# Kernel tuning notes

Hardware: AMD Instinct MI355X
Metric: run time of the kernel (lower is better)

Reference implementation:

```python
import jax, jax.numpy as jnp
import numpy as np

B, S, D = 2, 2048, 2048
H = 16
HD = D // H  # 128

def setup_inputs() -> dict:
    key = jax.random.key(0)
    k1, k2, k3 = jax.random.split(key, 3)
    x = jax.random.normal(k1, (B, S, D), dtype=jnp.float32)
    w_qkv = jax.random.normal(k2, (D, 3 * D), dtype=jnp.float32) * (1.0 / np.sqrt(D))
    b_qkv = jnp.zeros((3 * D,), dtype=jnp.float32)
    w_out = jax.random.normal(k3, (D, D), dtype=jnp.float32) * (1.0 / np.sqrt(D))
    b_out = jnp.zeros((D,), dtype=jnp.float32)
    return {"x": x, "w_qkv": w_qkv, "b_qkv": b_qkv, "w_out": w_out, "b_out": b_out}

def reference(x, w_qkv, b_qkv, w_out, b_out):
    batch, seq_len, channels = x.shape
    qkv = x @ w_qkv + b_qkv                      # [B,S,3D]
    q, k, v = jnp.split(qkv, 3, axis=-1)
    # [B,S,D] -> [B,H,S,HD]
    def heads(t):
        return t.reshape(batch, seq_len, H, HD).transpose(0, 2, 1, 3)
    q, k, v = heads(q), heads(k), heads(v)
    scale = 1.0 / np.sqrt(HD).astype(np.float32)
    attn = jnp.einsum('bhqd,bhkd->bhqk', q, k) * scale
    causal = jnp.tril(jnp.ones((seq_len, seq_len), dtype=bool))
    attn = jnp.where(causal, attn, -jnp.inf)
    attn = jax.nn.softmax(attn, axis=-1)
    y = jnp.einsum('bhqk,bhkd->bhqd', attn, v)   # [B,H,S,HD]
    y = y.transpose(0, 2, 1, 3).reshape(batch, seq_len, channels)
    return y @ w_out + b_out
```

## Files before the change

### kernel.cpp

```cpp
#include <hip/hip_runtime.h>
#include <hip/hip_bf16.h>
#include <cstdint>
#include <cstddef>

#define BB 2
#define SS 2048
#define DD 2048
#define HH 16
#define HDIM 128
#define QSCALE 0.12751743f

typedef short bf16x8 __attribute__((ext_vector_type(8)));
typedef float f32x4 __attribute__((ext_vector_type(4)));
typedef float f32x16 __attribute__((ext_vector_type(16)));

__device__ __forceinline__ ushort f2bf(float f) {
    union { float f; uint32_t u; } v; v.f = f;
    uint32_t u = v.u;
    u += 0x7fffu + ((u >> 16) & 1u);
    return (ushort)(u >> 16);
}

__device__ __forceinline__ ushort f2bf_fast(float f) {
    union { float f; uint32_t u; } v; v.f = f;
    return (ushort)((v.u + 0x8000u) >> 16);
}

__device__ __forceinline__ void gl16(const ushort* g, ushort* l) {
    __builtin_amdgcn_global_load_lds(
        (const __attribute__((address_space(1))) unsigned int*)g,
        (__attribute__((address_space(3))) unsigned int*)l,
        16, 0, 0);
}

__global__ __launch_bounds__(256) void cast_x_kernel(
    const float* __restrict__ X, ushort* __restrict__ Xb)
{
    size_t idx = ((size_t)blockIdx.x * 256 + threadIdx.x) * 8;
    float4 a = *(const float4*)(X + idx);
    float4 b = *(const float4*)(X + idx + 4);
    ushort4 o0, o1;
    o0.x = f2bf(a.x); o0.y = f2bf(a.y); o0.z = f2bf(a.z); o0.w = f2bf(a.w);
    o1.x = f2bf(b.x); o1.y = f2bf(b.y); o1.z = f2bf(b.z); o1.w = f2bf(b.w);
    *(ushort4*)(Xb + idx) = o0;
    *(ushort4*)(Xb + idx + 4) = o1;
}

__global__ __launch_bounds__(256) void transpose_cast_kernel(
    const float* __restrict__ W, ushort* __restrict__ Wt, int K, int N)
{
    __shared__ ushort tile[32][36];
    const int n0 = blockIdx.x * 32;
    const int k0 = blockIdx.y * 32;
    const int t = threadIdx.x;
    const int r = t >> 3;
    const int c = (t & 7) * 4;
    float4 a = *(const float4*)(W + (size_t)(k0 + r) * N + n0 + c);
    tile[r][c + 0] = f2bf(a.x); tile[r][c + 1] = f2bf(a.y);
    tile[r][c + 2] = f2bf(a.z); tile[r][c + 3] = f2bf(a.w);
    __syncthreads();
    ushort4 o;
    o.x = tile[c + 0][r]; o.y = tile[c + 1][r];
    o.z = tile[c + 2][r]; o.w = tile[c + 3][r];
    *(ushort4*)(Wt + (size_t)(n0 + r) * K + k0 + c) = o;
}

__global__ __launch_bounds__(256) void transpose_v_kernel(
    const ushort* __restrict__ V, ushort* __restrict__ Vt)
{
    __shared__ ushort tile[32][36];
    const int s0 = blockIdx.x * 32;
    const int h0 = blockIdx.y * 32;
    const int bh = blockIdx.z;
    const ushort* Vp = V + (size_t)bh * SS * HDIM;
    ushort* Vtp = Vt + (size_t)bh * HDIM * SS;
    const int t = threadIdx.x;
    const int r = t >> 3;
    const int c = (t & 7) * 4;
    *(ushort4*)&tile[r][c] = *(const ushort4*)(Vp + (size_t)(s0 + r) * HDIM + h0 + c);
    __syncthreads();
    ushort4 o;
    o.x = tile[c + 0][r]; o.y = tile[c + 1][r];
    o.z = tile[c + 2][r]; o.w = tile[c + 3][r];
    *(ushort4*)(Vtp + (size_t)(h0 + r) * SS + s0 + c) = o;
}

__global__ __launch_bounds__(256) void gemm_qkv_kernel(
    const ushort* __restrict__ A, const ushort* __restrict__ Bt,
    const float* __restrict__ bias,
    ushort* __restrict__ Qo, ushort* __restrict__ Ko, ushort* __restrict__ Vo)
{
    const int n0 = blockIdx.x * 128;
    const int m0 = blockIdx.y * 128;
    __shared__ ushort As[128 * 64];
    __shared__ ushort Bs[128 * 64];
    const int t = threadIdx.x, w = t >> 6, lane = t & 63;
    const int l31 = lane & 31, hh = lane >> 5;
    const int wr = w >> 1, wc = w & 1;
    const int l7 = l31 & 7;

    const int rt   = lane >> 3;
    const int koff = ((lane & 7) ^ rt) * 8;

    f32x16 acc[2][2];
#pragma unroll
    for (int i = 0; i < 2; ++i)
#pragma unroll
        for (int j = 0; j < 2; ++j) acc[i][j] = (f32x16)0.f;

    for (int k0 = 0; k0 < DD; k0 += 64) {
        __syncthreads();
#pragma unroll
        for (int q = 0; q < 4; ++q) {
            int R = (w * 4 + q) * 8 + rt;
            gl16(A  + (size_t)(m0 + R) * DD + k0 + koff, &As[(w * 4 + q) * 512]);
            gl16(Bt + (size_t)(n0 + R) * DD + k0 + koff, &Bs[(w * 4 + q) * 512]);
        }
        __syncthreads();
#pragma unroll
        for (int k16 = 0; k16 < 4; ++k16) {
            int lg = (k16 >> 1) * 4 + (k16 & 1) * 2 + hh;
            int co = (lg ^ l7) * 8;
            bf16x8 ar0 = *(const bf16x8*)&As[(wr * 64 + l31) * 64 + co];
            bf16x8 ar1 = *(const bf16x8*)&As[(wr * 64 + 32 + l31) * 64 + co];
            bf16x8 br0 = *(const bf16x8*)&Bs[(wc * 64 + l31) * 64 + co];
            bf16x8 br1 = *(const bf16x8*)&Bs[(wc * 64 + 32 + l31) * 64 + co];
            acc[0][0] = __builtin_amdgcn_mfma_f32_32x32x16_bf16(ar0, br0, acc[0][0], 0, 0, 0);
            acc[0][1] = __builtin_amdgcn_mfma_f32_32x32x16_bf16(ar0, br1, acc[0][1], 0, 0, 0);
            acc[1][0] = __builtin_amdgcn_mfma_f32_32x32x16_bf16(ar1, br0, acc[1][0], 0, 0, 0);
            acc[1][1] = __builtin_amdgcn_mfma_f32_32x32x16_bf16(ar1, br1, acc[1][1], 0, 0, 0);
        }
    }

    const int bidx = m0 >> 11;
    const int which = n0 >> 11;
    ushort* dst = (which == 0) ? Qo : ((which == 1) ? Ko : Vo);
    const float sc = (which == 0) ? QSCALE : 1.0f;
#pragma unroll
    for (int j = 0; j < 2; ++j) {
        int n = n0 + wc * 64 + j * 32 + l31;
        int c = n & 2047, h = c >> 7, hd = c & 127;
        float bv = bias[n];
        size_t base = ((size_t)(bidx * HH + h) * SS) * HDIM + hd;
#pragma unroll
        for (int i = 0; i < 2; ++i) {
#pragma unroll
            for (int r = 0; r < 16; ++r) {
                int s = (m0 & 2047) + wr * 64 + i * 32 + (r & 3) + 8 * (r >> 2) + 4 * hh;
                dst[base + (size_t)s * HDIM] = f2bf((acc[i][j][r] + bv) * sc);
            }
        }
    }
}

__global__ __launch_bounds__(256) void gemm_out_kernel(
    const ushort* __restrict__ A, const ushort* __restrict__ Bt,
    const float* __restrict__ bias, float* __restrict__ Out)
{
    const int n0 = blockIdx.x * 128;
    const int m0 = blockIdx.y * 128;
    __shared__ ushort As[128 * 64];
    __shared__ ushort Bs[128 * 64];
    const int t = threadIdx.x, w = t >> 6, lane = t & 63;
    const int l31 = lane & 31, hh = lane >> 5;
    const int wr = w >> 1, wc = w & 1;
    const int l7 = l31 & 7;

    const int rt   = lane >> 3;
    const int koff = ((lane & 7) ^ rt) * 8;

    f32x16 acc[2][2];
#pragma unroll
    for (int i = 0; i < 2; ++i)
#pragma unroll
        for (int j = 0; j < 2; ++j) acc[i][j] = (f32x16)0.f;

    for (int k0 = 0; k0 < DD; k0 += 64) {
        __syncthreads();
#pragma unroll
        for (int q = 0; q < 4; ++q) {
            int R = (w * 4 + q) * 8 + rt;
            gl16(A  + (size_t)(m0 + R) * DD + k0 + koff, &As[(w * 4 + q) * 512]);
            gl16(Bt + (size_t)(n0 + R) * DD + k0 + koff, &Bs[(w * 4 + q) * 512]);
        }
        __syncthreads();
#pragma unroll
        for (int k16 = 0; k16 < 4; ++k16) {
            int lg = (k16 >> 1) * 4 + (k16 & 1) * 2 + hh;
            int co = (lg ^ l7) * 8;
            bf16x8 ar0 = *(const bf16x8*)&As[(wr * 64 + l31) * 64 + co];
            bf16x8 ar1 = *(const bf16x8*)&As[(wr * 64 + 32 + l31) * 64 + co];
            bf16x8 br0 = *(const bf16x8*)&Bs[(wc * 64 + l31) * 64 + co];
            bf16x8 br1 = *(const bf16x8*)&Bs[(wc * 64 + 32 + l31) * 64 + co];
            acc[0][0] = __builtin_amdgcn_mfma_f32_32x32x16_bf16(ar0, br0, acc[0][0], 0, 0, 0);
            acc[0][1] = __builtin_amdgcn_mfma_f32_32x32x16_bf16(ar0, br1, acc[0][1], 0, 0, 0);
            acc[1][0] = __builtin_amdgcn_mfma_f32_32x32x16_bf16(ar1, br0, acc[1][0], 0, 0, 0);
            acc[1][1] = __builtin_amdgcn_mfma_f32_32x32x16_bf16(ar1, br1, acc[1][1], 0, 0, 0);
        }
    }

#pragma unroll
    for (int j = 0; j < 2; ++j) {
        int n = n0 + wc * 64 + j * 32 + l31;
        float bv = bias[n];
#pragma unroll
        for (int i = 0; i < 2; ++i) {
#pragma unroll
            for (int r = 0; r < 16; ++r) {
                int m = m0 + wr * 64 + i * 32 + (r & 3) + 8 * (r >> 2) + 4 * hh;
                Out[(size_t)m * DD + n] = acc[i][j][r] + bv;
            }
        }
    }
}

__global__ __launch_bounds__(256, 2) void attn_mfma_kernel(
    const ushort* __restrict__ Q, const ushort* __restrict__ K,
    const ushort* __restrict__ Vt, ushort* __restrict__ Y)
{
    const int fid = blockIdx.x;
    const int halfg = fid >> 8, rg = fid & 255;
    const int qt = halfg ? (rg & 15) : (15 - (rg & 15));
    const int bh = (halfg << 4) | (rg >> 4);
    const int q0 = qt * 128;
    const int b = bh >> 4, h = bh & 15;

    __shared__ ushort Ks[2][4 * 64 * 32];
    __shared__ ushort Vs[2][2 * 128 * 32];

    const int t = threadIdx.x, w = t >> 6, lane = t & 63;
    const int l31 = lane & 31, hh = lane >> 5;
    const int lrow = lane >> 2, lks = lane & 3;
    const int swst = (lrow >> 1) & 3;
    const int swr  = (l31 >> 1) & 3;

    const ushort* Qp = Q  + (size_t)bh * SS * HDIM;
    const ushort* Kp = K  + (size_t)bh * SS * HDIM;
    const ushort* Vp = Vt + (size_t)bh * HDIM * SS;

    bf16x8 aq[8];
#pragma unroll
    for (int kb2 = 0; kb2 < 8; ++kb2)
        aq[kb2] = *(const bf16x8*)(Qp + (size_t)(q0 + w * 32 + l31) * HDIM + kb2 * 16 + hh * 8);

    bf16x8 ones;
#pragma unroll
    for (int j = 0; j < 8; ++j) ones[j] = (short)0x3F80;

    f32x16 O[4];
#pragma unroll
    for (int nt = 0; nt < 4; ++nt) O[nt] = (f32x16)0.f;
    f32x16 Ol = (f32x16)0.f;

    const int kbdiag = 2 * qt + (w >> 1);
    const int nkb = 2 * qt + 2;
    const bool hi = (hh == 1);
    const int qg = q0 + w * 32 + l31;

#define STAGE_KV(kb_, s_) do {                                                  \
    const int kbase_ = (kb_) * 64;                                              \
    _Pragma("unroll")                                                           \
    for (int g = 0; g < 4; ++g) {                                               \
        int key = g * 16 + lrow;                                                \
        gl16(Kp + (size_t)(kbase_ + key) * HDIM + w * 32 + (lks ^ swst) * 8,    \
             &Ks[s_][w * 2048 + g * 512]);                                      \
    }                                                                           \
    _Pragma("unroll")                                                           \
    for (int g = 0; g < 4; ++g) {                                               \
        int pan = g >> 1, sub = g & 1;                                          \
        int dim = w * 32 + sub * 16 + lrow;                                     \
        gl16(Vp + (size_t)dim * SS + kbase_ + pan * 32 + (lks ^ swst) * 8,      \
             &Vs[s_][pan * 4096 + (w * 32 + sub * 16) * 32]);                   \
    }                                                                           \
} while (0)

    STAGE_KV(0, 0);

    for (int kb = 0; kb < nkb; ++kb) {
        const int kbase = kb * 64;
        const int slot = kb & 1;

        if (kb + 1 < nkb) {
            STAGE_KV(kb + 1, slot ^ 1);
            asm volatile("s_waitcnt vmcnt(8)" ::: "memory");
        } else {
            asm volatile("s_waitcnt vmcnt(0)" ::: "memory");
        }
        __builtin_amdgcn_s_barrier();

        const ushort* KsS = Ks[slot];
        const ushort* VsS = Vs[slot];

        if (kb <= kbdiag) {
            f32x16 st0 = (f32x16)0.f, st1 = (f32x16)0.f;
            __builtin_amdgcn_s_setprio(1);
#pragma unroll
            for (int kb2 = 0; kb2 < 8; ++kb2) {
                int co = (((kb2 & 1) * 2 + hh) ^ swr) * 8;
                bf16x8 bk0 = *(const bf16x8*)&KsS[(kb2 >> 1) * 2048 + l31 * 32 + co];
                bf16x8 bk1 = *(const bf16x8*)&KsS[(kb2 >> 1) * 2048 + (32 + l31) * 32 + co];
                st0 = __builtin_amdgcn_mfma_f32_32x32x16_bf16(bk0, aq[kb2], st0, 0, 0, 0);
                st1 = __builtin_amdgcn_mfma_f32_32x32x16_bf16(bk1, aq[kb2], st1, 0, 0, 0);
            }
            __builtin_amdgcn_s_setprio(0);

            if (kb == kbdiag) {
#pragma unroll
                for (int r = 0; r < 16; ++r) {
                    int keyr = kbase + (r & 3) + 8 * (r >> 2) + 4 * hh;
                    if (keyr > qg)      st0[r] = -1e30f;
                    if (keyr + 32 > qg) st1[r] = -1e30f;
                }
            }

#pragma unroll
            for (int half = 0; half < 2; ++half) {
                float p[16];
#pragma unroll
                for (int r = 0; r < 16; ++r)
                    p[r] = __builtin_amdgcn_exp2f((half == 0) ? st0[r] : st1[r]);
                uint w0[4], w1[4];
#pragma unroll
                for (int g = 0; g < 4; ++g) {
                    w0[g] = (uint)f2bf_fast(p[4 * g])
                          | ((uint)f2bf_fast(p[4 * g + 1]) << 16);
                    w1[g] = (uint)f2bf_fast(p[4 * g + 2])
                          | ((uint)f2bf_fast(p[4 * g + 3]) << 16);
                }
#pragma unroll
                for (int kblk2 = 0; kblk2 < 2; ++kblk2) {
                    uint own0 = hi ? w0[2 * kblk2 + 1] : w0[2 * kblk2];
                    uint own1 = hi ? w1[2 * kblk2 + 1] : w1[2 * kblk2];
                    uint snd0 = hi ? w0[2 * kblk2]     : w0[2 * kblk2 + 1];
                    uint snd1 = hi ? w1[2 * kblk2]     : w1[2 * kblk2 + 1];
                    uint ps0 = (uint)__shfl_xor((int)snd0, 32, 64);
                    uint ps1 = (uint)__shfl_xor((int)snd1, 32, 64);
                    union { uint u[4]; bf16x8 v; } fr;
                    fr.u[0] = hi ? ps0 : own0;
                    fr.u[1] = hi ? ps1 : own1;
                    fr.u[2] = hi ? own0 : ps0;
                    fr.u[3] = hi ? own1 : ps1;
                    int co = ((kblk2 * 2 + hh) ^ swr) * 8;
                    __builtin_amdgcn_s_setprio(1);
#pragma unroll
                    for (int nt = 0; nt < 4; ++nt) {
                        bf16x8 bv = *(const bf16x8*)&VsS[half * 4096 + (nt * 32 + l31) * 32 + co];
                        O[nt] = __builtin_amdgcn_mfma_f32_32x32x16_bf16(fr.v, bv, O[nt], 0, 0, 0);
                    }
                    Ol = __builtin_amdgcn_mfma_f32_32x32x16_bf16(fr.v, ones, Ol, 0, 0, 0);
                    __builtin_amdgcn_s_setprio(0);
                }
            }
        }
        __builtin_amdgcn_s_barrier();
    }
#undef STAGE_KV

#pragma unroll
    for (int r = 0; r < 16; ++r) {
        int s = q0 + w * 32 + (r & 3) + 8 * (r >> 2) + 4 * hh;
        float inv = 1.0f / Ol[r];
        size_t base = ((size_t)(b * SS + s)) * DD + h * HDIM;
#pragma unroll
        for (int nt = 0; nt < 4; ++nt)
            Y[base + nt * 32 + l31] = f2bf(O[nt][r] * inv);
    }
}

extern "C" void kernel_launch(void* const* d_in, const int* in_sizes, int n_in,
                              void* d_out, int out_size, void* d_ws, size_t ws_size,
                              hipStream_t stream) {
    const float* x     = (const float*)d_in[0];
    const float* w_qkv = (const float*)d_in[1];
    const float* b_qkv = (const float*)d_in[2];
    const float* w_out = (const float*)d_in[3];
    const float* b_out = (const float*)d_in[4];
    float* out = (float*)d_out;

    ushort* ws  = (ushort*)d_ws;
    ushort* xb  = ws;
    ushort* wtq = xb + 8388608;
    ushort* wto = wtq + 12582912;
    ushort* q   = wto + 4194304;
    ushort* k   = q + 8388608;
    ushort* v   = k + 8388608;
    ushort* vt  = v + 8388608;
    ushort* y   = vt + 8388608;

    cast_x_kernel<<<4096, 256, 0, stream>>>(x, xb);
    transpose_cast_kernel<<<dim3(192, 64), 256, 0, stream>>>(w_qkv, wtq, DD, 3 * DD);
    transpose_cast_kernel<<<dim3(64, 64), 256, 0, stream>>>(w_out, wto, DD, DD);
    gemm_qkv_kernel<<<dim3(48, 32), 256, 0, stream>>>(xb, wtq, b_qkv, q, k, v);
    transpose_v_kernel<<<dim3(64, 4, 32), 256, 0, stream>>>(v, vt);
    attn_mfma_kernel<<<dim3(512), 256, 0, stream>>>(q, k, vt, y);
    gemm_out_kernel<<<dim3(16, 32), 256, 0, stream>>>(y, wto, b_out, out);
}
```

Before: 373.2 us.

## Write V transposed directly from QKV GEMM epilogue and remap attention blocks to XCDs

```diff
diff --git a/kernel.cpp b/kernel.cpp
--- a/kernel.cpp
+++ b/kernel.cpp
@@ -65,26 +65,6 @@
     *(ushort4*)(Wt + (size_t)(n0 + r) * K + k0 + c) = o;
 }
 
-__global__ __launch_bounds__(256) void transpose_v_kernel(
-    const ushort* __restrict__ V, ushort* __restrict__ Vt)
-{
-    __shared__ ushort tile[32][36];
-    const int s0 = blockIdx.x * 32;
-    const int h0 = blockIdx.y * 32;
-    const int bh = blockIdx.z;
-    const ushort* Vp = V + (size_t)bh * SS * HDIM;
-    ushort* Vtp = Vt + (size_t)bh * HDIM * SS;
-    const int t = threadIdx.x;
-    const int r = t >> 3;
-    const int c = (t & 7) * 4;
-    *(ushort4*)&tile[r][c] = *(const ushort4*)(Vp + (size_t)(s0 + r) * HDIM + h0 + c);
-    __syncthreads();
-    ushort4 o;
-    o.x = tile[c + 0][r]; o.y = tile[c + 1][r];
-    o.z = tile[c + 2][r]; o.w = tile[c + 3][r];
-    *(ushort4*)(Vtp + (size_t)(h0 + r) * SS + s0 + c) = o;
-}
-
 __global__ __launch_bounds__(256) void gemm_qkv_kernel(
     const ushort* __restrict__ A, const ushort* __restrict__ Bt,
     const float* __restrict__ bias,
@@ -134,20 +114,43 @@
 
     const int bidx = m0 >> 11;
     const int which = n0 >> 11;
-    ushort* dst = (which == 0) ? Qo : ((which == 1) ? Ko : Vo);
-    const float sc = (which == 0) ? QSCALE : 1.0f;
-#pragma unroll
-    for (int j = 0; j < 2; ++j) {
-        int n = n0 + wc * 64 + j * 32 + l31;
-        int c = n & 2047, h = c >> 7, hd = c & 127;
-        float bv = bias[n];
-        size_t base = ((size_t)(bidx * HH + h) * SS) * HDIM + hd;
-#pragma unroll
-        for (int i = 0; i < 2; ++i) {
-#pragma unroll
-            for (int r = 0; r < 16; ++r) {
-                int s = (m0 & 2047) + wr * 64 + i * 32 + (r & 3) + 8 * (r >> 2) + 4 * hh;
-                dst[base + (size_t)s * HDIM] = f2bf((acc[i][j][r] + bv) * sc);
+    if (which == 2) {
+#pragma unroll
+        for (int j = 0; j < 2; ++j) {
+            int n = n0 + wc * 64 + j * 32 + l31;
+            int c = n & 2047, h = c >> 7, hd = c & 127;
+            float bv = bias[n];
+            size_t vbase = ((size_t)(bidx * HH + h) * HDIM + hd) * SS
+                         + (m0 & 2047) + wr * 64 + 4 * hh;
+#pragma unroll
+            for (int i = 0; i < 2; ++i) {
+#pragma unroll
+                for (int g = 0; g < 4; ++g) {
+                    ushort4 o;
+                    o.x = f2bf(acc[i][j][4 * g + 0] + bv);
+                    o.y = f2bf(acc[i][j][4 * g + 1] + bv);
+                    o.z = f2bf(acc[i][j][4 * g + 2] + bv);
+                    o.w = f2bf(acc[i][j][4 * g + 3] + bv);
+                    *(ushort4*)&Vo[vbase + i * 32 + 8 * g] = o;
+                }
+            }
+        }
+    } else {
+        ushort* dst = (which == 0) ? Qo : Ko;
+        const float sc = (which == 0) ? QSCALE : 1.0f;
+#pragma unroll
+        for (int j = 0; j < 2; ++j) {
+            int n = n0 + wc * 64 + j * 32 + l31;
+            int c = n & 2047, h = c >> 7, hd = c & 127;
+            float bv = bias[n];
+            size_t base = ((size_t)(bidx * HH + h) * SS) * HDIM + hd;
+#pragma unroll
+            for (int i = 0; i < 2; ++i) {
+#pragma unroll
+                for (int r = 0; r < 16; ++r) {
+                    int s = (m0 & 2047) + wr * 64 + i * 32 + (r & 3) + 8 * (r >> 2) + 4 * hh;
+                    dst[base + (size_t)s * HDIM] = f2bf((acc[i][j][r] + bv) * sc);
+                }
             }
         }
     }
@@ -219,9 +222,12 @@
     const ushort* __restrict__ Vt, ushort* __restrict__ Y)
 {
     const int fid = blockIdx.x;
-    const int halfg = fid >> 8, rg = fid & 255;
-    const int qt = halfg ? (rg & 15) : (15 - (rg & 15));
-    const int bh = (halfg << 4) | (rg >> 4);
+    const int xcd = fid & 7;
+    const int j   = fid >> 3;
+    const int bhsub = j >> 4;
+    const int bh  = bhsub * 8 + xcd;
+    const int jr  = j & 15;
+    const int qt  = (bhsub & 2) ? jr : (15 - jr);
     const int q0 = qt * 128;
     const int b = bh >> 4, h = bh & 15;
 
@@ -245,7 +251,7 @@
 
     bf16x8 ones;
 #pragma unroll
-    for (int j = 0; j < 8; ++j) ones[j] = (short)0x3F80;
+    for (int jj = 0; jj < 8; ++jj) ones[jj] = (short)0x3F80;
 
     f32x16 O[4];
 #pragma unroll
@@ -390,8 +396,7 @@
     cast_x_kernel<<<4096, 256, 0, stream>>>(x, xb);
     transpose_cast_kernel<<<dim3(192, 64), 256, 0, stream>>>(w_qkv, wtq, DD, 3 * DD);
     transpose_cast_kernel<<<dim3(64, 64), 256, 0, stream>>>(w_out, wto, DD, DD);
-    gemm_qkv_kernel<<<dim3(48, 32), 256, 0, stream>>>(xb, wtq, b_qkv, q, k, v);
-    transpose_v_kernel<<<dim3(64, 4, 32), 256, 0, stream>>>(v, vt);
+    gemm_qkv_kernel<<<dim3(48, 32), 256, 0, stream>>>(xb, wtq, b_qkv, q, k, vt);
     attn_mfma_kernel<<<dim3(512), 256, 0, stream>>>(q, k, vt, y);
     gemm_out_kernel<<<dim3(16, 32), 256, 0, stream>>>(y, wto, b_out, out);
 }
```

Result: no change. 368.3 us (-1.3%).
